# Kernel tuning notes

Hardware: AMD Instinct MI355X
Metric: run time of the kernel (lower is better)

## Reference

```python
import jax, jax.numpy as jnp
import numpy as np

NU = 1.0  # degrees of freedom of the Student-t / Tsallis softmax


def setup_inputs() -> dict:
    key = jax.random.key(0)
    k1, k2, k3, k4 = jax.random.split(key, 4)
    B, Nx, Nh, Ny = 8192, 2048, 512, 1024
    x = jax.random.normal(k1, (B, Nx), dtype=jnp.float32)
    W_fc = jax.random.normal(k2, (Nh, Nx), dtype=jnp.float32) * (1.0 / np.sqrt(Nx))
    b_fc = jax.random.normal(k3, (Nh,), dtype=jnp.float32) * 0.01
    W_q = jax.random.normal(k4, (Ny, Nh), dtype=jnp.float32) * (1.0 / np.sqrt(Nh))
    return {"x": x, "W_fc": W_fc, "b_fc": b_fc, "W_q": W_q}


def reference(x, W_fc, b_fc, W_q):
    # x: [B, Nx] -> relu -> Linear(Nx, Nh) -> relu
    h = jax.nn.relu(jax.nn.relu(x) @ W_fc.T + b_fc)  # [B, Nh]
    # Quadratic layer: squared Euclidean distance to each class prototype.
    # ||h - w_j||^2 = ||h||^2 - 2 h.w_j + ||w_j||^2  (avoids [B, Ny, Nh] tensor)
    d = (jnp.sum(h * h, axis=-1, keepdims=True)
         - 2.0 * (h @ W_q.T)
         + jnp.sum(W_q * W_q, axis=-1))  # [B, Ny]
    d = jnp.maximum(d, 0.0)  # guard tiny negatives from fp cancellation
    # LogTSoftmax: p_j \propto (1 + d_j/nu)^{-(nu+1)/2}
    t = (-(NU + 1.0) / 2.0) * jnp.log1p(d / NU)  # [B, Ny]
    return t - jax.scipy.special.logsumexp(t, axis=-1, keepdims=True)
```

## Files before the change

### kernel.cpp

```cpp
#include <hip/hip_runtime.h>
#include <stdint.h>
#include <stddef.h>

#define B_ROWS 8192
#define NX 2048
#define NH 512
#define NY 1024

#define X_ELEMS (B_ROWS * NX)
#define EW_ELEMS (X_ELEMS + NH * NX)
#define EW_BLOCKS (EW_ELEMS / (8 * 256))
#define WQ_BLOCKS (NY / 4)

typedef __attribute__((ext_vector_type(8))) short bf16x8;
typedef __attribute__((ext_vector_type(4))) float f32x4;

static __device__ __forceinline__ unsigned short f2bf(float f) {
    union { float f; unsigned int u; } c; c.f = f;
    unsigned int r = 0x7FFFu + ((c.u >> 16) & 1u);
    return (unsigned short)((c.u + r) >> 16);
}

static __device__ __forceinline__ void glld16(const void* g, void* l) {
    __builtin_amdgcn_global_load_lds(
        (const __attribute__((address_space(1))) unsigned int*)g,
        (__attribute__((address_space(3))) unsigned int*)l, 16, 0, 0);
}

__global__ __launch_bounds__(256) void prep_kernel(const float* __restrict__ x,
                                                   const float* __restrict__ wfc,
                                                   const float* __restrict__ wq,
                                                   unsigned short* __restrict__ xb,
                                                   unsigned short* __restrict__ wfcb,
                                                   unsigned short* __restrict__ wqb,
                                                   float* __restrict__ wqsq,
                                                   float* __restrict__ hsq) {
    const int bid = blockIdx.x;
    const int tid = threadIdx.x;
    if (bid < EW_BLOCKS) {
        size_t idx = ((size_t)bid * 256 + tid) * 8;
        if (idx < (size_t)X_ELEMS) {
            float4 a = *(const float4*)&x[idx];
            float4 b = *(const float4*)&x[idx + 4];
            bf16x8 o;
            o[0] = (short)f2bf(fmaxf(a.x, 0.f)); o[1] = (short)f2bf(fmaxf(a.y, 0.f));
            o[2] = (short)f2bf(fmaxf(a.z, 0.f)); o[3] = (short)f2bf(fmaxf(a.w, 0.f));
            o[4] = (short)f2bf(fmaxf(b.x, 0.f)); o[5] = (short)f2bf(fmaxf(b.y, 0.f));
            o[6] = (short)f2bf(fmaxf(b.z, 0.f)); o[7] = (short)f2bf(fmaxf(b.w, 0.f));
            *(bf16x8*)&xb[idx] = o;
        } else {
            size_t off = idx - X_ELEMS;
            float4 a = *(const float4*)&wfc[off];
            float4 b = *(const float4*)&wfc[off + 4];
            bf16x8 o;
            o[0] = (short)f2bf(a.x); o[1] = (short)f2bf(a.y);
            o[2] = (short)f2bf(a.z); o[3] = (short)f2bf(a.w);
            o[4] = (short)f2bf(b.x); o[5] = (short)f2bf(b.y);
            o[6] = (short)f2bf(b.z); o[7] = (short)f2bf(b.w);
            *(bf16x8*)&wfcb[off] = o;
        }
    } else {
        const int b2 = bid - EW_BLOCKS;
        const int lane = tid & 63;
        const int row = b2 * 4 + (tid >> 6);
        const float* p = wq + (size_t)row * NH + lane * 8;
        float4 a = *(const float4*)p;
        float4 b = *(const float4*)(p + 4);
        bf16x8 o;
        o[0] = (short)f2bf(a.x); o[1] = (short)f2bf(a.y);
        o[2] = (short)f2bf(a.z); o[3] = (short)f2bf(a.w);
        o[4] = (short)f2bf(b.x); o[5] = (short)f2bf(b.y);
        o[6] = (short)f2bf(b.z); o[7] = (short)f2bf(b.w);
        *(bf16x8*)&wqb[(size_t)row * NH + lane * 8] = o;
        float s = a.x*a.x + a.y*a.y + a.z*a.z + a.w*a.w
                + b.x*b.x + b.y*b.y + b.z*b.z + b.w*b.w;
        #pragma unroll
        for (int off = 32; off > 0; off >>= 1) s += __shfl_xor(s, off);
        if (lane == 0) wqsq[row] = s;
        if (tid < 32) hsq[b2 * 32 + tid] = 0.0f;
    }
}

__global__ __launch_bounds__(512, 2) void gemm1_kernel(const unsigned short* __restrict__ xb,
                                                       const unsigned short* __restrict__ wfcb,
                                                       const float* __restrict__ b_fc,
                                                       unsigned short* __restrict__ hb,
                                                       float* __restrict__ hsq) {
    __shared__ unsigned char smem[65536];
    unsigned char* AsB = smem;
    unsigned char* BsB = smem + 32768;

    const int tid = threadIdx.x;
    const int lane = tid & 63;
    const int grp = tid >> 8;
    const int wave = (tid >> 6) & 3;
    const int wm = wave >> 1, wn = wave & 1;
    const int quad = lane >> 4;
    const int r = lane & 15;

    const int bid = blockIdx.x;
    const int n0 = ((bid >> 3) & 3) * 128;
    const int m0 = (((bid & 7) << 3) | (bid >> 5)) * 128;
    const int kbase = grp * (NX / 2);

    f32x4 acc[4][4];
    #pragma unroll
    for (int i = 0; i < 4; ++i)
        #pragma unroll
        for (int j = 0; j < 4; ++j) acc[i][j] = (f32x4)(0.0f);

    const int lrow = lane >> 2;
    const int gch = (lane & 3) ^ ((lrow >> 1) & 3);
    const char* xbB = (const char*)xb;
    const char* wfB = (const char*)wfcb;
    const int fsw = (quad ^ ((r >> 1) & 3)) * 16;

    auto stage = [&](int buf, int k0) {
        const int sb = grp * 16384 + buf * 8192;
        #pragma unroll
        for (int c = 0; c < 2; ++c) {
            int R0 = wave * 32 + c * 16;
            glld16(xbB + (size_t)(m0 + R0 + lrow) * (NX * 2) + k0 * 2 + gch * 16,
                   AsB + sb + R0 * 64);
            glld16(wfB + (size_t)(n0 + R0 + lrow) * (NX * 2) + k0 * 2 + gch * 16,
                   BsB + sb + R0 * 64);
        }
    };

    stage(0, kbase);
    #pragma unroll 1
    for (int it = 0; it < 32; ++it) {
        __syncthreads();
        if (it + 1 < 32) stage((it + 1) & 1, kbase + it * 32 + 32);
        const unsigned char* ab = AsB + grp * 16384 + (it & 1) * 8192;
        const unsigned char* bb = BsB + grp * 16384 + (it & 1) * 8192;
        bf16x8 af[4], bfv[4];
        #pragma unroll
        for (int i = 0; i < 4; ++i)
            af[i] = *(const bf16x8*)(ab + (wm * 64 + i * 16 + r) * 64 + fsw);
        #pragma unroll
        for (int j = 0; j < 4; ++j)
            bfv[j] = *(const bf16x8*)(bb + (wn * 64 + j * 16 + r) * 64 + fsw);
        #pragma unroll
        for (int i = 0; i < 4; ++i)
            #pragma unroll
            for (int j = 0; j < 4; ++j)
                acc[i][j] = __builtin_amdgcn_mfma_f32_16x16x32_bf16(af[i], bfv[j], acc[i][j], 0, 0, 0);
    }

    float* smemF = (float*)smem;
    __syncthreads();
    if (grp == 1) {
        #pragma unroll
        for (int i = 0; i < 4; ++i) {
            #pragma unroll
            for (int j = 0; j < 4; ++j) {
                int cl = wn * 64 + j * 16 + r;
                int rowb = wm * 64 + i * 16 + quad * 4;
                *(f32x4*)(smemF + cl * 128 + (rowb ^ ((cl & 7) << 2))) = acc[i][j];
            }
        }
    }
    __syncthreads();
    if (grp == 0) {
        float p[4][4];
        #pragma unroll
        for (int i = 0; i < 4; ++i)
            #pragma unroll
            for (int rr = 0; rr < 4; ++rr) p[i][rr] = 0.0f;

        #pragma unroll
        for (int i = 0; i < 4; ++i) {
            #pragma unroll
            for (int j = 0; j < 4; ++j) {
                int cl = wn * 64 + j * 16 + r;
                int rowb = wm * 64 + i * 16 + quad * 4;
                f32x4 o = *(const f32x4*)(smemF + cl * 128 + (rowb ^ ((cl & 7) << 2)));
                int col = n0 + cl;
                float bias = b_fc[col];
                #pragma unroll
                for (int rr = 0; rr < 4; ++rr) {
                    float v = fmaxf(acc[i][j][rr] + o[rr] + bias, 0.0f);
                    hb[(size_t)(m0 + rowb + rr) * NH + col] = f2bf(v);
                    p[i][rr] += v * v;
                }
            }
        }
        #pragma unroll
        for (int mask = 1; mask < 16; mask <<= 1) {
            #pragma unroll
            for (int i = 0; i < 4; ++i)
                #pragma unroll
                for (int rr = 0; rr < 4; ++rr)
                    p[i][rr] += __shfl_xor(p[i][rr], mask);
        }
        if (r == 0) {
            #pragma unroll
            for (int i = 0; i < 4; ++i)
                #pragma unroll
                for (int rr = 0; rr < 4; ++rr)
                    atomicAdd(&hsq[m0 + wm * 64 + i * 16 + quad * 4 + rr], p[i][rr]);
        }
    }
}

__global__ __launch_bounds__(512, 2) void gemm2_kernel(const unsigned short* __restrict__ hb,
                                                       const unsigned short* __restrict__ wqb,
                                                       const float* __restrict__ hsq,
                                                       const float* __restrict__ wqsq,
                                                       float* __restrict__ out) {
    __shared__ unsigned char smem[135168];
    char* AsB = (char*)smem;
    char* BsB = (char*)smem + 4096;

    const int tid = threadIdx.x;
    const int lane = tid & 63;
    const int wave = tid >> 6;
    const int quad = lane >> 4;
    const int r = lane & 15;
    const int m0 = blockIdx.x * 32;

    f32x4 acc[2][8];
    #pragma unroll
    for (int i = 0; i < 2; ++i)
        #pragma unroll
        for (int j = 0; j < 8; ++j) acc[i][j] = (f32x4)(0.0f);

    const int lrow = lane >> 2;
    const int gch = (lane & 3) ^ ((lrow >> 1) & 3);
    const char* bsrc = (const char*)wqb + (size_t)(wave * 128 + lrow) * (NH * 2) + gch * 16;
    const char* asrc = (const char*)hb + (size_t)(m0 + wave * 16 + lrow) * (NH * 2) + gch * 16;
    const int fsw = (quad ^ ((r >> 1) & 3)) * 16;

    auto stage = [&](int buf, int k0) {
        #pragma unroll
        for (int c = 0; c < 8; ++c)
            glld16(bsrc + (size_t)k0 * 2 + c * 16384,
                   BsB + buf * 65536 + wave * 8192 + c * 1024);
        if (wave < 2)
            glld16(asrc + (size_t)k0 * 2, AsB + buf * 2048 + wave * 1024);
    };

    stage(0, 0);
    #pragma unroll 1
    for (int it = 0; it < NH / 32; ++it) {
        __syncthreads();
        if (it + 1 < NH / 32) stage((it + 1) & 1, it * 32 + 32);
        const char* ab = AsB + (it & 1) * 2048;
        const char* bb = BsB + (it & 1) * 65536 + wave * 8192;
        bf16x8 af[2], bfv[8];
        #pragma unroll
        for (int i = 0; i < 2; ++i)
            af[i] = *(const bf16x8*)(ab + (i * 16 + r) * 64 + fsw);
        #pragma unroll
        for (int j = 0; j < 8; ++j)
            bfv[j] = *(const bf16x8*)(bb + (j * 16 + r) * 64 + fsw);
        #pragma unroll
        for (int i = 0; i < 2; ++i)
            #pragma unroll
            for (int j = 0; j < 8; ++j)
                acc[i][j] = __builtin_amdgcn_mfma_f32_16x16x32_bf16(af[i], bfv[j], acc[i][j], 0, 0, 0);
    }

    float hs_[2][4];
    #pragma unroll
    for (int i = 0; i < 2; ++i)
        #pragma unroll
        for (int rr = 0; rr < 4; ++rr)
            hs_[i][rr] = hsq[m0 + i * 16 + quad * 4 + rr];

    float srow[2][4];
    #pragma unroll
    for (int i = 0; i < 2; ++i)
        #pragma unroll
        for (int rr = 0; rr < 4; ++rr) srow[i][rr] = 0.0f;

    #pragma unroll
    for (int j = 0; j < 8; ++j) {
        float wqv = wqsq[wave * 128 + j * 16 + r];
        #pragma unroll
        for (int i = 0; i < 2; ++i) {
            #pragma unroll
            for (int rr = 0; rr < 4; ++rr) {
                float d = hs_[i][rr] - 2.0f * acc[i][j][rr] + wqv;
                d = fmaxf(d, 0.0f);
                float onepd = 1.0f + d;
                srow[i][rr] += __builtin_amdgcn_rcpf(onepd);
                acc[i][j][rr] = -__logf(onepd);
            }
        }
    }
    #pragma unroll
    for (int mask = 1; mask < 16; mask <<= 1)
        #pragma unroll
        for (int i = 0; i < 2; ++i)
            #pragma unroll
            for (int rr = 0; rr < 4; ++rr)
                srow[i][rr] += __shfl_xor(srow[i][rr], mask);

    float* smemF = (float*)smem;
    __syncthreads();
    if (r == 0) {
        #pragma unroll
        for (int i = 0; i < 2; ++i)
            #pragma unroll
            for (int rr = 0; rr < 4; ++rr)
                smemF[wave * 32 + i * 16 + quad * 4 + rr] = srow[i][rr];
    }
    __syncthreads();
    if (tid < 32) {
        float S = 0.0f;
        #pragma unroll
        for (int w = 0; w < 8; ++w) S += smemF[w * 32 + tid];
        smemF[256 + tid] = __logf(S);
    }
    __syncthreads();

    #pragma unroll
    for (int i = 0; i < 2; ++i) {
        #pragma unroll
        for (int rr = 0; rr < 4; ++rr) {
            float l = smemF[256 + i * 16 + quad * 4 + rr];
            size_t rowoff = (size_t)(m0 + i * 16 + quad * 4 + rr) * NY + wave * 128 + r;
            #pragma unroll
            for (int j = 0; j < 8; ++j)
                out[rowoff + j * 16] = acc[i][j][rr] - l;
        }
    }
}

extern "C" void kernel_launch(void* const* d_in, const int* in_sizes, int n_in,
                              void* d_out, int out_size, void* d_ws, size_t ws_size,
                              hipStream_t stream) {
    const float* x    = (const float*)d_in[0];
    const float* W_fc = (const float*)d_in[1];
    const float* b_fc = (const float*)d_in[2];
    const float* W_q  = (const float*)d_in[3];
    float* out = (float*)d_out;

    char* ws = (char*)d_ws;
    unsigned short* xb   = (unsigned short*)(ws);
    unsigned short* wfcb = (unsigned short*)(ws + 33554432);
    unsigned short* wqb  = (unsigned short*)(ws + 35651584);
    float*          wqsq = (float*)(ws + 36700160);
    unsigned short* hb   = (unsigned short*)(ws + 36704256);
    float*          hsq  = (float*)(ws + 45092864);

    prep_kernel<<<EW_BLOCKS + WQ_BLOCKS, 256, 0, stream>>>(x, W_fc, W_q, xb, wfcb, wqb, wqsq, hsq);
    gemm1_kernel<<<256, 512, 0, stream>>>(xb, wfcb, b_fc, hb, hsq);
    gemm2_kernel<<<B_ROWS / 32, 512, 0, stream>>>(hb, wqb, hsq, wqsq, out);
}
```

Before: 173.2 us.

## Shrink GEMM tiles and shared memory to raise occupancy, drop split-K

gemm1 drops its intra-block split-K and the cross-group reduction through shared memory. It now uses 128x64 tiles with 2x2 MFMA fragments per wave over 512 blocks, using less LDS and launch bounds that allow 4 blocks per CU. gemm2 moves from double-buffered to single-buffered LDS, halving shared memory so more blocks can be resident. In exchange, load/compute overlap within a block is lost and data reuse per tile drops, so global and LDS traffic per FLOP rise.

Result: slower. 177.7 us (+2.6%).

```diff
diff --git a/kernel.cpp b/kernel.cpp
--- a/kernel.cpp
+++ b/kernel.cpp
@@ -81,137 +81,113 @@
     }
 }
 
-__global__ __launch_bounds__(512, 2) void gemm1_kernel(const unsigned short* __restrict__ xb,
+__global__ __launch_bounds__(512, 4) void gemm1_kernel(const unsigned short* __restrict__ xb,
                                                        const unsigned short* __restrict__ wfcb,
                                                        const float* __restrict__ b_fc,
                                                        unsigned short* __restrict__ hb,
                                                        float* __restrict__ hsq) {
-    __shared__ unsigned char smem[65536];
+    __shared__ unsigned char smem[24576];
     unsigned char* AsB = smem;
-    unsigned char* BsB = smem + 32768;
+    unsigned char* BsB = smem + 16384;
 
     const int tid = threadIdx.x;
     const int lane = tid & 63;
-    const int grp = tid >> 8;
-    const int wave = (tid >> 6) & 3;
-    const int wm = wave >> 1, wn = wave & 1;
+    const int wave = tid >> 6;
+    const int wm = wave & 3;
+    const int wn = wave >> 2;
     const int quad = lane >> 4;
     const int r = lane & 15;
 
     const int bid = blockIdx.x;
-    const int n0 = ((bid >> 3) & 3) * 128;
-    const int m0 = (((bid & 7) << 3) | (bid >> 5)) * 128;
-    const int kbase = grp * (NX / 2);
-
-    f32x4 acc[4][4];
-    #pragma unroll
-    for (int i = 0; i < 4; ++i)
-        #pragma unroll
-        for (int j = 0; j < 4; ++j) acc[i][j] = (f32x4)(0.0f);
+    const int c_ = bid & 7, q_ = bid >> 3;
+    const int n0 = (q_ & 7) * 64;
+    const int m0 = ((c_ << 3) | (q_ >> 3)) * 128;
+
+    f32x4 acc[2][2];
+    #pragma unroll
+    for (int i = 0; i < 2; ++i)
+        #pragma unroll
+        for (int j = 0; j < 2; ++j) acc[i][j] = (f32x4)(0.0f);
 
     const int lrow = lane >> 2;
     const int gch = (lane & 3) ^ ((lrow >> 1) & 3);
-    const char* xbB = (const char*)xb;
-    const char* wfB = (const char*)wfcb;
     const int fsw = (quad ^ ((r >> 1) & 3)) * 16;
 
+    const char* asrc = (const char*)xb + (size_t)(m0 + wave * 16 + lrow) * (NX * 2) + gch * 16;
+    const char* bsrc = (const char*)wfcb + (size_t)(n0 + (wave & 3) * 16 + lrow) * (NX * 2) + gch * 16;
+
     auto stage = [&](int buf, int k0) {
-        const int sb = grp * 16384 + buf * 8192;
-        #pragma unroll
-        for (int c = 0; c < 2; ++c) {
-            int R0 = wave * 32 + c * 16;
-            glld16(xbB + (size_t)(m0 + R0 + lrow) * (NX * 2) + k0 * 2 + gch * 16,
-                   AsB + sb + R0 * 64);
-            glld16(wfB + (size_t)(n0 + R0 + lrow) * (NX * 2) + k0 * 2 + gch * 16,
-                   BsB + sb + R0 * 64);
-        }
+        glld16(asrc + (size_t)k0 * 2, AsB + buf * 8192 + wave * 1024);
+        if (wave < 4)
+            glld16(bsrc + (size_t)k0 * 2, BsB + buf * 4096 + wave * 1024);
     };
 
-    stage(0, kbase);
+    stage(0, 0);
     #pragma unroll 1
-    for (int it = 0; it < 32; ++it) {
+    for (int it = 0; it < NX / 32; ++it) {
         __syncthreads();
-        if (it + 1 < 32) stage((it + 1) & 1, kbase + it * 32 + 32);
-        const unsigned char* ab = AsB + grp * 16384 + (it & 1) * 8192;
-        const unsigned char* bb = BsB + grp * 16384 + (it & 1) * 8192;
-        bf16x8 af[4], bfv[4];
-        #pragma unroll
-        for (int i = 0; i < 4; ++i)
-            af[i] = *(const bf16x8*)(ab + (wm * 64 + i * 16 + r) * 64 + fsw);
-        #pragma unroll
-        for (int j = 0; j < 4; ++j)
-            bfv[j] = *(const bf16x8*)(bb + (wn * 64 + j * 16 + r) * 64 + fsw);
-        #pragma unroll
-        for (int i = 0; i < 4; ++i)
-            #pragma unroll
-            for (int j = 0; j < 4; ++j)
+        if (it + 1 < NX / 32) stage((it + 1) & 1, it * 32 + 32);
+        const unsigned char* ab = AsB + (it & 1) * 8192;
+        const unsigned char* bb = BsB + (it & 1) * 4096;
+        bf16x8 af[2], bfv[2];
+        #pragma unroll
+        for (int i = 0; i < 2; ++i)
+            af[i] = *(const bf16x8*)(ab + (wm * 32 + i * 16 + r) * 64 + fsw);
+        #pragma unroll
+        for (int j = 0; j < 2; ++j)
+            bfv[j] = *(const bf16x8*)(bb + (wn * 32 + j * 16 + r) * 64 + fsw);
+        #pragma unroll
+        for (int i = 0; i < 2; ++i)
+            #pragma unroll
+            for (int j = 0; j < 2; ++j)
                 acc[i][j] = __builtin_amdgcn_mfma_f32_16x16x32_bf16(af[i], bfv[j], acc[i][j], 0, 0, 0);
     }
 
-    float* smemF = (float*)smem;
-    __syncthreads();
-    if (grp == 1) {
-        #pragma unroll
-        for (int i = 0; i < 4; ++i) {
-            #pragma unroll
-            for (int j = 0; j < 4; ++j) {
-                int cl = wn * 64 + j * 16 + r;
-                int rowb = wm * 64 + i * 16 + quad * 4;
-                *(f32x4*)(smemF + cl * 128 + (rowb ^ ((cl & 7) << 2))) = acc[i][j];
+    float p[2][4];
+    #pragma unroll
+    for (int i = 0; i < 2; ++i)
+        #pragma unroll
+        for (int rr = 0; rr < 4; ++rr) p[i][rr] = 0.0f;
+
+    #pragma unroll
+    for (int j = 0; j < 2; ++j) {
+        int col = n0 + wn * 32 + j * 16 + r;
+        float bias = b_fc[col];
+        #pragma unroll
+        for (int i = 0; i < 2; ++i) {
+            int rowb = m0 + wm * 32 + i * 16 + quad * 4;
+            #pragma unroll
+            for (int rr = 0; rr < 4; ++rr) {
+                float v = fmaxf(acc[i][j][rr] + bias, 0.0f);
+                hb[(size_t)(rowb + rr) * NH + col] = f2bf(v);
+                p[i][rr] += v * v;
             }
         }
     }
-    __syncthreads();
-    if (grp == 0) {
-        float p[4][4];
-        #pragma unroll
-        for (int i = 0; i < 4; ++i)
-            #pragma unroll
-            for (int rr = 0; rr < 4; ++rr) p[i][rr] = 0.0f;
-
-        #pragma unroll
-        for (int i = 0; i < 4; ++i) {
-            #pragma unroll
-            for (int j = 0; j < 4; ++j) {
-                int cl = wn * 64 + j * 16 + r;
-                int rowb = wm * 64 + i * 16 + quad * 4;
-                f32x4 o = *(const f32x4*)(smemF + cl * 128 + (rowb ^ ((cl & 7) << 2)));
-                int col = n0 + cl;
-                float bias = b_fc[col];
-                #pragma unroll
-                for (int rr = 0; rr < 4; ++rr) {
-                    float v = fmaxf(acc[i][j][rr] + o[rr] + bias, 0.0f);
-                    hb[(size_t)(m0 + rowb + rr) * NH + col] = f2bf(v);
-                    p[i][rr] += v * v;
-                }
-            }
-        }
-        #pragma unroll
-        for (int mask = 1; mask < 16; mask <<= 1) {
-            #pragma unroll
-            for (int i = 0; i < 4; ++i)
-                #pragma unroll
-                for (int rr = 0; rr < 4; ++rr)
-                    p[i][rr] += __shfl_xor(p[i][rr], mask);
-        }
-        if (r == 0) {
-            #pragma unroll
-            for (int i = 0; i < 4; ++i)
-                #pragma unroll
-                for (int rr = 0; rr < 4; ++rr)
-                    atomicAdd(&hsq[m0 + wm * 64 + i * 16 + quad * 4 + rr], p[i][rr]);
-        }
-    }
-}
-
-__global__ __launch_bounds__(512, 2) void gemm2_kernel(const unsigned short* __restrict__ hb,
+    #pragma unroll
+    for (int mask = 1; mask < 16; mask <<= 1)
+        #pragma unroll
+        for (int i = 0; i < 2; ++i)
+            #pragma unroll
+            for (int rr = 0; rr < 4; ++rr)
+                p[i][rr] += __shfl_xor(p[i][rr], mask);
+    if (r == 0) {
+        #pragma unroll
+        for (int i = 0; i < 2; ++i)
+            #pragma unroll
+            for (int rr = 0; rr < 4; ++rr)
+                atomicAdd(&hsq[m0 + wm * 32 + i * 16 + quad * 4 + rr], p[i][rr]);
+    }
+}
+
+__global__ __launch_bounds__(512, 4) void gemm2_kernel(const unsigned short* __restrict__ hb,
                                                        const unsigned short* __restrict__ wqb,
                                                        const float* __restrict__ hsq,
                                                        const float* __restrict__ wqsq,
                                                        float* __restrict__ out) {
-    __shared__ unsigned char smem[135168];
-    char* AsB = (char*)smem;
-    char* BsB = (char*)smem + 4096;
+    __shared__ unsigned char smem[67584];
+    char* BsB = (char*)smem;
+    char* AsB = (char*)smem + 65536;
 
     const int tid = threadIdx.x;
     const int lane = tid & 63;
@@ -228,38 +204,41 @@
 
     const int lrow = lane >> 2;
     const int gch = (lane & 3) ^ ((lrow >> 1) & 3);
+    const int fsw = (quad ^ ((r >> 1) & 3)) * 16;
+
     const char* bsrc = (const char*)wqb + (size_t)(wave * 128 + lrow) * (NH * 2) + gch * 16;
     const char* asrc = (const char*)hb + (size_t)(m0 + wave * 16 + lrow) * (NH * 2) + gch * 16;
-    const int fsw = (quad ^ ((r >> 1) & 3)) * 16;
-
-    auto stage = [&](int buf, int k0) {
+
+    auto stage = [&](int k0) {
         #pragma unroll
         for (int c = 0; c < 8; ++c)
-            glld16(bsrc + (size_t)k0 * 2 + c * 16384,
-                   BsB + buf * 65536 + wave * 8192 + c * 1024);
+            glld16(bsrc + (size_t)(c * 16 * NH + k0) * 2,
+                   BsB + (wave * 128 + c * 16) * 64);
         if (wave < 2)
-            glld16(asrc + (size_t)k0 * 2, AsB + buf * 2048 + wave * 1024);
+            glld16(asrc + (size_t)k0 * 2, AsB + wave * 1024);
     };
 
-    stage(0, 0);
     #pragma unroll 1
     for (int it = 0; it < NH / 32; ++it) {
+        stage(it * 32);
         __syncthreads();
-        if (it + 1 < NH / 32) stage((it + 1) & 1, it * 32 + 32);
-        const char* ab = AsB + (it & 1) * 2048;
-        const char* bb = BsB + (it & 1) * 65536 + wave * 8192;
-        bf16x8 af[2], bfv[8];
-        #pragma unroll
-        for (int i = 0; i < 2; ++i)
-            af[i] = *(const bf16x8*)(ab + (i * 16 + r) * 64 + fsw);
-        #pragma unroll
-        for (int j = 0; j < 8; ++j)
-            bfv[j] = *(const bf16x8*)(bb + (j * 16 + r) * 64 + fsw);
-        #pragma unroll
-        for (int i = 0; i < 2; ++i)
-            #pragma unroll
-            for (int j = 0; j < 8; ++j)
-                acc[i][j] = __builtin_amdgcn_mfma_f32_16x16x32_bf16(af[i], bfv[j], acc[i][j], 0, 0, 0);
+        bf16x8 af[2];
+        #pragma unroll
+        for (int i = 0; i < 2; ++i)
+            af[i] = *(const bf16x8*)(AsB + (i * 16 + r) * 64 + fsw);
+        #pragma unroll
+        for (int jh = 0; jh < 2; ++jh) {
+            bf16x8 bfv[4];
+            #pragma unroll
+            for (int j = 0; j < 4; ++j)
+                bfv[j] = *(const bf16x8*)(BsB + (wave * 128 + jh * 64 + j * 16 + r) * 64 + fsw);
+            #pragma unroll
+            for (int i = 0; i < 2; ++i)
+                #pragma unroll
+                for (int j = 0; j < 4; ++j)
+                    acc[i][jh * 4 + j] = __builtin_amdgcn_mfma_f32_16x16x32_bf16(af[i], bfv[j], acc[i][jh * 4 + j], 0, 0, 0);
+        }
+        __syncthreads();
     }
 
     float hs_[2][4];
@@ -347,6 +326,6 @@
     float*          hsq  = (float*)(ws + 45092864);
 
     prep_kernel<<<EW_BLOCKS + WQ_BLOCKS, 256, 0, stream>>>(x, W_fc, W_q, xb, wfcb, wqb, wqsq, hsq);
-    gemm1_kernel<<<256, 512, 0, stream>>>(xb, wfcb, b_fc, hb, hsq);
+    gemm1_kernel<<<512, 512, 0, stream>>>(xb, wfcb, b_fc, hb, hsq);
     gemm2_kernel<<<B_ROWS / 32, 512, 0, stream>>>(hb, wqb, hsq, wqsq, out);
 }
```
